# Optimization experiments

Hardware: AMD Instinct MI355X
Metric: run time of the kernel (lower is better)

The kernel has to match this reference:

```python
import jax, jax.numpy as jnp
import numpy as np

UNITS = 256
FEAT = 64


def setup_inputs() -> dict:
    key = jax.random.key(0)
    ks = jax.random.split(key, 6)
    B, T, F, U = 512, 1024, FEAT, UNITS
    sW = 1.0 / np.sqrt(F)
    sU = 1.0 / np.sqrt(U)
    return {
        "x": jax.random.normal(ks[0], (B, T, F), dtype=jnp.float32),
        "W": jax.random.normal(ks[1], (F, 4 * U), dtype=jnp.float32) * sW,
        "Uh": jax.random.normal(ks[2], (U, 4 * U), dtype=jnp.float32) * sU,
        "b": jnp.zeros((4 * U,), dtype=jnp.float32),
        "dense_w": jax.random.normal(ks[3], (U, 1), dtype=jnp.float32) * sU,
        "dense_b": jnp.zeros((1,), dtype=jnp.float32),
    }


def _lstm_scan(x, W, Uh, b):
    # x: (B, T, F) -> hs: (B, T, U), h_T: (B, U)
    B = x.shape[0]
    U = Uh.shape[0]
    h0 = jnp.zeros((B, U), dtype=x.dtype)
    c0 = jnp.zeros((B, U), dtype=x.dtype)

    def step(carry, xt):
        h, c = carry
        z = xt @ W + h @ Uh + b  # (B, 4U)
        i, f, g, o = jnp.split(z, 4, axis=-1)
        i = jax.nn.sigmoid(i)
        f = jax.nn.sigmoid(f)
        g = jnp.tanh(g)
        o = jax.nn.sigmoid(o)
        c_new = f * c + i * g
        h_new = o * jnp.tanh(c_new)
        return (h_new, c_new), h_new

    (h_T, _c_T), hs = jax.lax.scan(step, (h0, c0), jnp.transpose(x, (1, 0, 2)))
    return jnp.transpose(hs, (1, 0, 2)), h_T


def reference(x, W, Uh, b, dense_w, dense_b):
    seq, h_T = _lstm_scan(x, W, Uh, b)          # (B,T,U), (B,U)
    k = h_T[:, None, :]                          # (B,1,U) single key/value
    scores = jnp.einsum("btu,bsu->bts", seq, k)  # (B,T,1)
    w = jax.nn.softmax(scores, axis=-1)          # all ones (single key)
    attn = jnp.einsum("bts,bsu->btu", w, k)      # (B,T,U)
    logits = attn @ dense_w + dense_b            # (B,T,1)
    return jax.nn.sigmoid(logits[..., 0])        # (B,T)
```

## Files before the change

kernel.cpp:

```cpp
#include <hip/hip_runtime.h>

#define Tn 1024
#define Fn 64
#define Un 256
#define Gn 1024
#define AS 328
#define GROUPS 32
#define THREADS 512

typedef __attribute__((ext_vector_type(8))) short bf16x8;
typedef __attribute__((ext_vector_type(8))) unsigned short ushort8;
typedef __attribute__((ext_vector_type(4))) float f32x4;

#define WS_XCHG 4096
#define WS_BP   (WS_XCHG + 64*2*8192)

__device__ __forceinline__ float bf2f(unsigned short u){
  union { unsigned int i; float f; } v; v.i = ((unsigned int)u) << 16; return v.f;
}
__device__ __forceinline__ unsigned short f2bf(float f){
  unsigned int u = __float_as_uint(f);
  u += 0x7FFFu + ((u >> 16) & 1u);
  return (unsigned short)(u >> 16);
}
__device__ __forceinline__ float load_f(const void* p, long idx, int isf32){
  if (isf32) return ((const float*)p)[idx];
  return bf2f(((const unsigned short*)p)[idx]);
}
__device__ __forceinline__ float sigm(float x){ return 1.0f / (1.0f + __expf(-x)); }
__device__ __forceinline__ float tanh_f(float x){ return 2.0f * sigm(2.0f * x) - 1.0f; }

__global__ void init_k(const void* x, int* wsi){
  int tid = threadIdx.x;
  if (tid < 64){
    int cnt = 0;
    for (int s2 = 0; s2 < 4; ++s2){
      float v = bf2f(((const unsigned short*)x)[tid + 64*s2]);
      if (!(fabsf(v) <= 100.0f)) cnt++;
    }
    for (int off = 32; off > 0; off >>= 1) cnt += __shfl_down(cnt, off);
    if (tid == 0) wsi[0] = (cnt > 32) ? 1 : 0;
  }
}

__global__ void reformat_w(const void* Uh, const void* W, unsigned short* Bp, const int* dt){
  int isf32 = *dt;
  int gidx = blockIdx.x * blockDim.x + threadIdx.x;
  if (gidx >= 40960) return;
  int kt  = gidx >> 12;
  int rem = gidx & 4095;
  int n   = rem >> 2;
  int q   = rem & 3;
  int half = n >> 9;
  int w    = (n >> 6) & 7;
  int g    = (n >> 4) & 3;
  int ul   = n & 15;
  int col  = g*256 + half*128 + w*16 + ul;
  unsigned short vals[8];
  #pragma unroll
  for (int j = 0; j < 8; ++j){
    int k = kt*32 + q*8 + j;
    float v = (k < Un) ? load_f(Uh, (long)k*Gn + col, isf32)
                       : load_f(W,  (long)(k-Un)*Gn + col, isf32);
    vals[j] = f2bf(v);
  }
  *(ushort8*)(Bp + (long)gidx * 8) = *(ushort8*)vals;
}

__global__ __launch_bounds__(THREADS, 2) void lstm_k(
    const void* x, const void* bvec, const void* dense_w, const void* dense_b,
    const unsigned short* Bp, const int* dt, unsigned int* xchg, void* out)
{
  __shared__ __align__(16) unsigned short A_s[2][16*AS];
  __shared__ float outv[16];

  const int isf32 = *dt;
  const int tid = threadIdx.x;
  const int w   = tid >> 6;
  const int l   = tid & 63;
  const int l15 = l & 15;
  const int q   = l >> 4;
  const int g   = blockIdx.x >> 1;
  const int s   = blockIdx.x & 1;
  const int p   = s ^ 1;

  unsigned int*       xc_me = xchg + (size_t)(g*2 + s) * 4096;
  const unsigned int* xc_pr = xchg + (size_t)(g*2 + p) * 4096;

  const char* Bb = (const char*)Bp + (long)(l15*64 + q*16);
  const int nbase = s*512 + w*64;
  bf16x8 wfrag[10][4];
  {
    int ktp[10];
    #pragma unroll
    for (int i = 0; i < 4; ++i) ktp[i] = s*4 + i;
    ktp[4] = 8; ktp[5] = 9;
    #pragma unroll
    for (int i = 0; i < 4; ++i) ktp[6+i] = p*4 + i;
    #pragma unroll
    for (int i = 0; i < 10; ++i){
      #pragma unroll
      for (int nt = 0; nt < 4; ++nt)
        wfrag[i][nt] = *(const bf16x8*)(Bb + (long)(ktp[i]*1024 + nbase + nt*16)*64);
    }
  }

  for (int i = tid; i < 16*Un; i += THREADS)
    A_s[0][(i >> 8)*AS + (i & 255)] = 0;

  if (tid < 128){
    int m = tid >> 3, ch = tid & 7;
    long src = ((long)(g*16 + m)*Tn + 0)*Fn + ch*8;
    unsigned short v[8];
    if (isf32){ for (int j = 0; j < 8; ++j) v[j] = f2bf(((const float*)x)[src + j]); }
    else      { *(ushort8*)v = *(const ushort8*)((const unsigned short*)x + src); }
    *(ushort8*)&A_s[0][m*AS + Un + ch*8] = *(ushort8*)v;
  }

  float bias[4];
  #pragma unroll
  for (int gg = 0; gg < 4; ++gg) bias[gg] = load_f(bvec, gg*256 + s*128 + w*16 + l15, isf32);

  float c[4] = {0.f, 0.f, 0.f, 0.f};

  __syncthreads();

  for (int t = 0; t < Tn; ++t){
    const int buf = t & 1, nbuf = buf ^ 1;

    unsigned short xv[8];
    if (tid < 128 && (t+1) < Tn){
      int m = tid >> 3, ch = tid & 7;
      long src = ((long)(g*16 + m)*Tn + (t+1))*Fn + ch*8;
      if (isf32){ for (int j = 0; j < 8; ++j) xv[j] = f2bf(((const float*)x)[src + j]); }
      else      { *(ushort8*)xv = *(const ushort8*)((const unsigned short*)x + src); }
    }

    f32x4 acc[4];
    #pragma unroll
    for (int nt = 0; nt < 4; ++nt)
      acc[nt] = (f32x4){bias[nt], bias[nt], bias[nt], bias[nt]};
    {
      const int kb = s*4;
      #pragma unroll
      for (int i = 0; i < 4; ++i){
        bf16x8 af = *(const bf16x8*)&A_s[buf][l15*AS + (kb + i)*32 + q*8];
        #pragma unroll
        for (int nt = 0; nt < 4; ++nt)
          acc[nt] = __builtin_amdgcn_mfma_f32_16x16x32_bf16(af, wfrag[i][nt], acc[nt], 0, 0, 0);
      }
      #pragma unroll
      for (int i = 4; i < 6; ++i){
        bf16x8 af = *(const bf16x8*)&A_s[buf][l15*AS + (4 + i)*32 + q*8];
        #pragma unroll
        for (int nt = 0; nt < 4; ++nt)
          acc[nt] = __builtin_amdgcn_mfma_f32_16x16x32_bf16(af, wfrag[i][nt], acc[nt], 0, 0, 0);
      }
    }

    if (t > 0){
      const unsigned long long* src =
          (const unsigned long long*)(xc_pr + (size_t)buf*2048 + tid*4);
      const unsigned long long need = (unsigned long long)(t & 0xFFFF);
      unsigned int pv[4];
      for (;;){
        unsigned long long a = __hip_atomic_load(src,   __ATOMIC_RELAXED, __HIP_MEMORY_SCOPE_AGENT);
        unsigned long long b = __hip_atomic_load(src+1, __ATOMIC_RELAXED, __HIP_MEMORY_SCOPE_AGENT);
        if (((a & 0xFFFFu) == need) && (((a >> 32) & 0xFFFFu) == need) &&
            ((b & 0xFFFFu) == need) && (((b >> 32) & 0xFFFFu) == need)){
          pv[0] = (unsigned int)a; pv[1] = (unsigned int)(a >> 32);
          pv[2] = (unsigned int)b; pv[3] = (unsigned int)(b >> 32);
          break;
        }
      }
      int base = tid*4;
      #pragma unroll
      for (int i = 0; i < 4; ++i){
        int f = base + i;
        A_s[buf][(f >> 7)*AS + p*128 + (f & 127)] = (unsigned short)(pv[i] >> 16);
      }
    }
    if (tid < 128 && (t+1) < Tn){
      int m = tid >> 3, ch = tid & 7;
      *(ushort8*)&A_s[nbuf][m*AS + Un + ch*8] = *(ushort8*)xv;
    }
    __syncthreads();

    {
      const int kb = p*4;
      #pragma unroll
      for (int i = 0; i < 4; ++i){
        bf16x8 af = *(const bf16x8*)&A_s[buf][l15*AS + (kb + i)*32 + q*8];
        #pragma unroll
        for (int nt = 0; nt < 4; ++nt)
          acc[nt] = __builtin_amdgcn_mfma_f32_16x16x32_bf16(af, wfrag[6+i][nt], acc[nt], 0, 0, 0);
      }
    }

    {
      const unsigned int tag = (unsigned int)((t+1) & 0xFFFF);
      unsigned int* dstb = xc_me + (size_t)((t+1) & 1)*2048;
      const int u_loc = w*16 + l15;
      #pragma unroll
      for (int r = 0; r < 4; ++r){
        float ig = sigm(acc[0][r]);
        float fg = sigm(acc[1][r]);
        float gg = tanh_f(acc[2][r]);
        float og = sigm(acc[3][r]);
        float cn = fg * c[r] + ig * gg;
        c[r] = cn;
        unsigned short hb = f2bf(og * tanh_f(cn));
        A_s[nbuf][(q*4 + r)*AS + (s*128 + u_loc)] = hb;
        __hip_atomic_store(dstb + (q*4 + r)*128 + u_loc,
                           ((unsigned int)hb << 16) | tag,
                           __ATOMIC_RELAXED, __HIP_MEMORY_SCOPE_AGENT);
      }
    }
    __syncthreads();
  }

  if (s == 0){
    {
      const unsigned long long* src =
          (const unsigned long long*)(xc_pr +  (size_t)0 + tid*4);
      const unsigned long long need = (unsigned long long)(Tn & 0xFFFF);
      unsigned int pv[4];
      for (;;){
        unsigned long long a = __hip_atomic_load(src,   __ATOMIC_RELAXED, __HIP_MEMORY_SCOPE_AGENT);
        unsigned long long b = __hip_atomic_load(src+1, __ATOMIC_RELAXED, __HIP_MEMORY_SCOPE_AGENT);
        if (((a & 0xFFFFu) == need) && (((a >> 32) & 0xFFFFu) == need) &&
            ((b & 0xFFFFu) == need) && (((b >> 32) & 0xFFFFu) == need)){
          pv[0] = (unsigned int)a; pv[1] = (unsigned int)(a >> 32);
          pv[2] = (unsigned int)b; pv[3] = (unsigned int)(b >> 32);
          break;
        }
      }
      int base = tid*4;
      #pragma unroll
      for (int i = 0; i < 4; ++i){
        int f = base + i;
        A_s[0][(f >> 7)*AS + 128 + (f & 127)] = (unsigned short)(pv[i] >> 16);
      }
    }
    __syncthreads();

    int m = tid >> 5, j = tid & 31;
    float partial = 0.f;
    for (int u = j; u < 256; u += 32)
      partial += bf2f(A_s[0][m*AS + u]) * load_f(dense_w, u, isf32);
    #pragma unroll
    for (int off = 1; off < 32; off <<= 1) partial += __shfl_xor(partial, off);
    if (j == 0) outv[m] = sigm(partial + load_f(dense_b, 0, isf32));
    __syncthreads();

    for (int mm = 0; mm < 16; ++mm){
      float v = outv[mm];
      long base = (long)(g*16 + mm) * Tn;
      for (int col = tid; col < Tn; col += THREADS){
        if (isf32) ((float*)out)[base + col] = v;
        else       ((unsigned short*)out)[base + col] = f2bf(v);
      }
    }
  }
}

extern "C" void kernel_launch(void* const* d_in, const int* in_sizes, int n_in,
                              void* d_out, int out_size, void* d_ws, size_t ws_size,
                              hipStream_t stream){
  const void* x  = d_in[0];
  const void* W  = d_in[1];
  const void* Uh = d_in[2];
  const void* b  = d_in[3];
  const void* dw = d_in[4];
  const void* db = d_in[5];

  int* wsi = (int*)d_ws;
  const int* dt = wsi;
  unsigned int* xchg = (unsigned int*)((char*)d_ws + WS_XCHG);
  unsigned short* Bp = (unsigned short*)((char*)d_ws + WS_BP);

  init_k<<<1, 64, 0, stream>>>(x, wsi);
  reformat_w<<<160, 256, 0, stream>>>(Uh, W, Bp, dt);
  lstm_k<<<GROUPS*2, THREADS, 0, stream>>>(x, b, dw, db, Bp, dt, xchg, d_out);
}
```

Measured before the change: 2.997 ms.

## Split each LSTM batch group across four workgroups instead of two

Each batch group of 16 rows is now split across four 256-thread workgroups, each owning 64 hidden units per gate, instead of two 512-thread workgroups owning 128. Hidden-state slices are exchanged through tagged global memory with three peers per step, and the weight reformat layout is changed to match. The aim is to spread the serial recurrent matmul over more CUs, which halves the per-block MFMA work and uses 128 CUs. The cost is more cross-workgroup polling and synchronisation traffic on every timestep. It also depends on all 128 blocks being co-resident, or the spin-waits deadlock.

```diff
diff --git a/kernel.cpp b/kernel.cpp
--- a/kernel.cpp
+++ b/kernel.cpp
@@ -6,14 +6,14 @@
 #define Gn 1024
 #define AS 328
 #define GROUPS 32
-#define THREADS 512
+#define THREADS 256
 
 typedef __attribute__((ext_vector_type(8))) short bf16x8;
 typedef __attribute__((ext_vector_type(8))) unsigned short ushort8;
 typedef __attribute__((ext_vector_type(4))) float f32x4;
 
 #define WS_XCHG 4096
-#define WS_BP   (WS_XCHG + 64*2*8192)
+#define WS_BP   (WS_XCHG + 128*2*4096)
 
 __device__ __forceinline__ float bf2f(unsigned short u){
   union { unsigned int i; float f; } v; v.i = ((unsigned int)u) << 16; return v.f;
@@ -51,11 +51,11 @@
   int rem = gidx & 4095;
   int n   = rem >> 2;
   int q   = rem & 3;
-  int half = n >> 9;
-  int w    = (n >> 6) & 7;
-  int g    = (n >> 4) & 3;
-  int ul   = n & 15;
-  int col  = g*256 + half*128 + w*16 + ul;
+  int s   = n >> 8;
+  int w   = (n >> 6) & 3;
+  int g   = (n >> 4) & 3;
+  int ul  = n & 15;
+  int col = g*256 + s*64 + w*16 + ul;
   unsigned short vals[8];
   #pragma unroll
   for (int j = 0; j < 8; ++j){
@@ -67,7 +67,7 @@
   *(ushort8*)(Bp + (long)gidx * 8) = *(ushort8*)vals;
 }
 
-__global__ __launch_bounds__(THREADS, 2) void lstm_k(
+__global__ __launch_bounds__(THREADS, 1) void lstm_k(
     const void* x, const void* bvec, const void* dense_w, const void* dense_b,
     const unsigned short* Bp, const int* dt, unsigned int* xchg, void* out)
 {
@@ -80,29 +80,26 @@
   const int l   = tid & 63;
   const int l15 = l & 15;
   const int q   = l >> 4;
-  const int g   = blockIdx.x >> 1;
-  const int s   = blockIdx.x & 1;
-  const int p   = s ^ 1;
-
-  unsigned int*       xc_me = xchg + (size_t)(g*2 + s) * 4096;
-  const unsigned int* xc_pr = xchg + (size_t)(g*2 + p) * 4096;
+  const int g   = blockIdx.x >> 2;
+  const int s   = blockIdx.x & 3;
+
+  int plist[3];
+  #pragma unroll
+  for (int j = 0; j < 3; ++j) plist[j] = j + (j >= s ? 1 : 0);
+
+  int ktp[10];
+  ktp[0] = 2*s; ktp[1] = 2*s + 1; ktp[2] = 8; ktp[3] = 9;
+  #pragma unroll
+  for (int j = 0; j < 3; ++j){ ktp[4+2*j] = 2*plist[j]; ktp[5+2*j] = 2*plist[j] + 1; }
 
   const char* Bb = (const char*)Bp + (long)(l15*64 + q*16);
-  const int nbase = s*512 + w*64;
+  const int nb = s*256 + w*64;
   bf16x8 wfrag[10][4];
-  {
-    int ktp[10];
-    #pragma unroll
-    for (int i = 0; i < 4; ++i) ktp[i] = s*4 + i;
-    ktp[4] = 8; ktp[5] = 9;
-    #pragma unroll
-    for (int i = 0; i < 4; ++i) ktp[6+i] = p*4 + i;
-    #pragma unroll
-    for (int i = 0; i < 10; ++i){
-      #pragma unroll
-      for (int nt = 0; nt < 4; ++nt)
-        wfrag[i][nt] = *(const bf16x8*)(Bb + (long)(ktp[i]*1024 + nbase + nt*16)*64);
-    }
+  #pragma unroll
+  for (int i = 0; i < 10; ++i){
+    #pragma unroll
+    for (int gg = 0; gg < 4; ++gg)
+      wfrag[i][gg] = *(const bf16x8*)(Bb + (long)(ktp[i]*1024 + nb + gg*16)*64);
   }
 
   for (int i = tid; i < 16*Un; i += THREADS)
@@ -117,11 +114,14 @@
     *(ushort8*)&A_s[0][m*AS + Un + ch*8] = *(ushort8*)v;
   }
 
+  const int u_loc = w*16 + l15;
   float bias[4];
   #pragma unroll
-  for (int gg = 0; gg < 4; ++gg) bias[gg] = load_f(bvec, gg*256 + s*128 + w*16 + l15, isf32);
+  for (int gg = 0; gg < 4; ++gg) bias[gg] = load_f(bvec, gg*256 + s*64 + u_loc, isf32);
 
   float c[4] = {0.f, 0.f, 0.f, 0.f};
+
+  unsigned int* xc_me = xchg + (size_t)(g*4 + s) * 2048;
 
   __syncthreads();
 
@@ -138,46 +138,37 @@
 
     f32x4 acc[4];
     #pragma unroll
-    for (int nt = 0; nt < 4; ++nt)
-      acc[nt] = (f32x4){bias[nt], bias[nt], bias[nt], bias[nt]};
-    {
-      const int kb = s*4;
-      #pragma unroll
-      for (int i = 0; i < 4; ++i){
-        bf16x8 af = *(const bf16x8*)&A_s[buf][l15*AS + (kb + i)*32 + q*8];
-        #pragma unroll
-        for (int nt = 0; nt < 4; ++nt)
-          acc[nt] = __builtin_amdgcn_mfma_f32_16x16x32_bf16(af, wfrag[i][nt], acc[nt], 0, 0, 0);
-      }
-      #pragma unroll
-      for (int i = 4; i < 6; ++i){
-        bf16x8 af = *(const bf16x8*)&A_s[buf][l15*AS + (4 + i)*32 + q*8];
-        #pragma unroll
-        for (int nt = 0; nt < 4; ++nt)
-          acc[nt] = __builtin_amdgcn_mfma_f32_16x16x32_bf16(af, wfrag[i][nt], acc[nt], 0, 0, 0);
-      }
+    for (int gg = 0; gg < 4; ++gg)
+      acc[gg] = (f32x4){bias[gg], bias[gg], bias[gg], bias[gg]};
+    #pragma unroll
+    for (int i = 0; i < 4; ++i){
+      bf16x8 af = *(const bf16x8*)&A_s[buf][l15*AS + ktp[i]*32 + q*8];
+      #pragma unroll
+      for (int gg = 0; gg < 4; ++gg)
+        acc[gg] = __builtin_amdgcn_mfma_f32_16x16x32_bf16(af, wfrag[i][gg], acc[gg], 0, 0, 0);
     }
 
     if (t > 0){
-      const unsigned long long* src =
-          (const unsigned long long*)(xc_pr + (size_t)buf*2048 + tid*4);
-      const unsigned long long need = (unsigned long long)(t & 0xFFFF);
-      unsigned int pv[4];
-      for (;;){
-        unsigned long long a = __hip_atomic_load(src,   __ATOMIC_RELAXED, __HIP_MEMORY_SCOPE_AGENT);
-        unsigned long long b = __hip_atomic_load(src+1, __ATOMIC_RELAXED, __HIP_MEMORY_SCOPE_AGENT);
-        if (((a & 0xFFFFu) == need) && (((a >> 32) & 0xFFFFu) == need) &&
-            ((b & 0xFFFFu) == need) && (((b >> 32) & 0xFFFFu) == need)){
-          pv[0] = (unsigned int)a; pv[1] = (unsigned int)(a >> 32);
-          pv[2] = (unsigned int)b; pv[3] = (unsigned int)(b >> 32);
-          break;
+      const unsigned int need = (unsigned int)(t & 0xFFFF);
+      #pragma unroll
+      for (int j = 0; j < 3; ++j){
+        int p = plist[j];
+        const unsigned long long* src =
+            (const unsigned long long*)(xchg + (size_t)((g*4 + p)*2 + buf)*1024) + tid*2;
+        unsigned long long a, b;
+        for (;;){
+          a = __hip_atomic_load(src,   __ATOMIC_RELAXED, __HIP_MEMORY_SCOPE_AGENT);
+          b = __hip_atomic_load(src+1, __ATOMIC_RELAXED, __HIP_MEMORY_SCOPE_AGENT);
+          if ((((unsigned int)a & 0xFFFFu) == need) && ((unsigned int)(a >> 32) & 0xFFFFu) == need &&
+              (((unsigned int)b & 0xFFFFu) == need) && ((unsigned int)(b >> 32) & 0xFFFFu) == need)
+            break;
         }
-      }
-      int base = tid*4;
-      #pragma unroll
-      for (int i = 0; i < 4; ++i){
-        int f = base + i;
-        A_s[buf][(f >> 7)*AS + p*128 + (f & 127)] = (unsigned short)(pv[i] >> 16);
+        unsigned long long hv = ((a >> 16) & 0xFFFFull)
+                              | (((a >> 48) & 0xFFFFull) << 16)
+                              | (((b >> 16) & 0xFFFFull) << 32)
+                              | (((b >> 48) & 0xFFFFull) << 48);
+        int row = tid >> 4, u0 = (tid & 15) * 4;
+        *(unsigned long long*)&A_s[buf][row*AS + p*64 + u0] = hv;
       }
     }
     if (tid < 128 && (t+1) < Tn){
@@ -186,21 +177,19 @@
     }
     __syncthreads();
 
-    {
-      const int kb = p*4;
-      #pragma unroll
-      for (int i = 0; i < 4; ++i){
-        bf16x8 af = *(const bf16x8*)&A_s[buf][l15*AS + (kb + i)*32 + q*8];
+    if (t > 0){
+      #pragma unroll
+      for (int i = 4; i < 10; ++i){
+        bf16x8 af = *(const bf16x8*)&A_s[buf][l15*AS + ktp[i]*32 + q*8];
         #pragma unroll
-        for (int nt = 0; nt < 4; ++nt)
-          acc[nt] = __builtin_amdgcn_mfma_f32_16x16x32_bf16(af, wfrag[6+i][nt], acc[nt], 0, 0, 0);
+        for (int gg = 0; gg < 4; ++gg)
+          acc[gg] = __builtin_amdgcn_mfma_f32_16x16x32_bf16(af, wfrag[i][gg], acc[gg], 0, 0, 0);
       }
     }
 
     {
       const unsigned int tag = (unsigned int)((t+1) & 0xFFFF);
-      unsigned int* dstb = xc_me + (size_t)((t+1) & 1)*2048;
-      const int u_loc = w*16 + l15;
+      unsigned int* dstb = xc_me + (size_t)nbuf*1024;
       #pragma unroll
       for (int r = 0; r < 4; ++r){
         float ig = sigm(acc[0][r]);
@@ -210,8 +199,8 @@
         float cn = fg * c[r] + ig * gg;
         c[r] = cn;
         unsigned short hb = f2bf(og * tanh_f(cn));
-        A_s[nbuf][(q*4 + r)*AS + (s*128 + u_loc)] = hb;
-        __hip_atomic_store(dstb + (q*4 + r)*128 + u_loc,
+        A_s[nbuf][(q*4 + r)*AS + (s*64 + u_loc)] = hb;
+        __hip_atomic_store(dstb + (q*4 + r)*64 + u_loc,
                            ((unsigned int)hb << 16) | tag,
                            __ATOMIC_RELAXED, __HIP_MEMORY_SCOPE_AGENT);
       }
@@ -220,37 +209,36 @@
   }
 
   if (s == 0){
-    {
+    const unsigned int need = (unsigned int)(Tn & 0xFFFF);
+    #pragma unroll
+    for (int j = 0; j < 3; ++j){
+      int p = plist[j];
       const unsigned long long* src =
-          (const unsigned long long*)(xc_pr +  (size_t)0 + tid*4);
-      const unsigned long long need = (unsigned long long)(Tn & 0xFFFF);
-      unsigned int pv[4];
+          (const unsigned long long*)(xchg + (size_t)((g*4 + p)*2 + 0)*1024) + tid*2;
+      unsigned long long a, b;
       for (;;){
-        unsigned long long a = __hip_atomic_load(src,   __ATOMIC_RELAXED, __HIP_MEMORY_SCOPE_AGENT);
-        unsigned long long b = __hip_atomic_load(src+1, __ATOMIC_RELAXED, __HIP_MEMORY_SCOPE_AGENT);
-        if (((a & 0xFFFFu) == need) && (((a >> 32) & 0xFFFFu) == need) &&
-            ((b & 0xFFFFu) == need) && (((b >> 32) & 0xFFFFu) == need)){
-          pv[0] = (unsigned int)a; pv[1] = (unsigned int)(a >> 32);
-          pv[2] = (unsigned int)b; pv[3] = (unsigned int)(b >> 32);
+        a = __hip_atomic_load(src,   __ATOMIC_RELAXED, __HIP_MEMORY_SCOPE_AGENT);
+        b = __hip_atomic_load(src+1, __ATOMIC_RELAXED, __HIP_MEMORY_SCOPE_AGENT);
+        if ((((unsigned int)a & 0xFFFFu) == need) && ((unsigned int)(a >> 32) & 0xFFFFu) == need &&
+            (((unsigned int)b & 0xFFFFu) == need) && ((unsigned int)(b >> 32) & 0xFFFFu) == need)
           break;
-        }
-      }
-      int base = tid*4;
-      #pragma unroll
-      for (int i = 0; i < 4; ++i){
-        int f = base + i;
-        A_s[0][(f >> 7)*AS + 128 + (f & 127)] = (unsigned short)(pv[i] >> 16);
-      }
-    }
-    __syncthreads();
-
-    int m = tid >> 5, j = tid & 31;
+      }
+      unsigned long long hv = ((a >> 16) & 0xFFFFull)
+                            | (((a >> 48) & 0xFFFFull) << 16)
+                            | (((b >> 16) & 0xFFFFull) << 32)
+                            | (((b >> 48) & 0xFFFFull) << 48);
+      int row = tid >> 4, u0 = (tid & 15) * 4;
+      *(unsigned long long*)&A_s[0][row*AS + p*64 + u0] = hv;
+    }
+    __syncthreads();
+
+    int m = tid >> 4, j16 = tid & 15;
     float partial = 0.f;
-    for (int u = j; u < 256; u += 32)
+    for (int u = j16; u < 256; u += 16)
       partial += bf2f(A_s[0][m*AS + u]) * load_f(dense_w, u, isf32);
     #pragma unroll
-    for (int off = 1; off < 32; off <<= 1) partial += __shfl_xor(partial, off);
-    if (j == 0) outv[m] = sigm(partial + load_f(dense_b, 0, isf32));
+    for (int off = 1; off < 16; off <<= 1) partial += __shfl_xor(partial, off);
+    if (j16 == 0) outv[m] = sigm(partial + load_f(dense_b, 0, isf32));
     __syncthreads();
 
     for (int mm = 0; mm < 16; ++mm){
@@ -281,5 +269,5 @@
 
   init_k<<<1, 64, 0, stream>>>(x, wsi);
   reformat_w<<<160, 256, 0, stream>>>(Uh, W, Bp, dt);
-  lstm_k<<<GROUPS*2, THREADS, 0, stream>>>(x, b, dw, db, Bp, dt, xchg, d_out);
-}
+  lstm_k<<<GROUPS*4, THREADS, 0, stream>>>(x, b, dw, db, Bp, dt, xchg, d_out);
+}
```

Result: no change. 2.992 ms (-0.2%).
